# Kernel tuning notes

Hardware: AMD Instinct MI355X
Metric: run time of the kernel (lower is better)

Reference implementation:

```python
import jax, jax.numpy as jnp
import numpy as np

D_MODEL = 768
N_HEADS = 12
D_HEAD = D_MODEL // N_HEADS

def setup_inputs() -> dict:
    key = jax.random.key(0)
    ks = jax.random.split(key, 5)
    B, T = 2, 4096
    x = jax.random.normal(ks[0], (B, T, D_MODEL), dtype=jnp.float32)
    s_in = 1.0 / np.sqrt(D_MODEL)
    W_qkv = jax.random.normal(ks[1], (D_MODEL, 3 * D_MODEL), dtype=jnp.float32) * s_in
    b_qkv = jnp.zeros((3 * D_MODEL,), dtype=jnp.float32)
    W_proj = jax.random.normal(ks[2], (D_MODEL, D_MODEL), dtype=jnp.float32) * s_in
    b_proj = jnp.zeros((D_MODEL,), dtype=jnp.float32)
    return {"x": x, "W_qkv": W_qkv, "b_qkv": b_qkv, "W_proj": W_proj, "b_proj": b_proj}

def reference(x, W_qkv, b_qkv, W_proj, b_proj):
    B, T, C = x.shape
    qkv = x @ W_qkv + b_qkv                      # [B,T,3C]
    q, k, v = jnp.split(qkv, 3, axis=-1)
    def heads(t):
        return t.reshape(B, T, N_HEADS, D_HEAD).transpose(0, 2, 1, 3)  # [B,H,T,d]
    q, k, v = heads(q), heads(k), heads(v)
    scale = 1.0 / np.sqrt(D_HEAD)
    att = jnp.einsum('bhqd,bhkd->bhqk', q, k) * scale  # [B,H,T,T]
    causal = jnp.tril(jnp.ones((T, T), dtype=bool))
    att = jnp.where(causal[None, None], att, -jnp.inf)
    att = jax.nn.softmax(att, axis=-1)
    y = jnp.einsum('bhqk,bhkd->bhqd', att, v)          # [B,H,T,d]
    y = y.transpose(0, 2, 1, 3).reshape(B, T, C)
    return y @ W_proj + b_proj
```

## Files before the change

kernel.cpp:

```cpp
#include <hip/hip_runtime.h>
#include <hip/hip_bf16.h>

typedef __bf16 bf16_t;
typedef bf16_t bf16x4 __attribute__((ext_vector_type(4)));
typedef bf16_t bf16x8 __attribute__((ext_vector_type(8)));
typedef float  f32x4  __attribute__((ext_vector_type(4)));

#define TSEQ   4096
#define NBATCH 2
#define DMODEL 768
#define NHEADS 12
#define DHEAD  64
#define NTOK   (NBATCH*TSEQ)
#define NQKV   (3*DMODEL)

#define QSCALE 0.18033688011112042f
#define SMAX 24.0f

__device__ __forceinline__ f32x4 mfma16(bf16x8 a, bf16x8 b, f32x4 c) {
  return __builtin_amdgcn_mfma_f32_16x16x32_bf16(a, b, c, 0, 0, 0);
}

__device__ __forceinline__ void glds16(const bf16_t* g, bf16_t* l) {
  __builtin_amdgcn_global_load_lds(
      (const __attribute__((address_space(1))) void*)g,
      (__attribute__((address_space(3))) void*)l, 16, 0, 0);
}
__device__ __forceinline__ void glds16f(const float* g, float* l) {
  __builtin_amdgcn_global_load_lds(
      (const __attribute__((address_space(1))) void*)g,
      (__attribute__((address_space(3))) void*)l, 16, 0, 0);
}

__global__ __launch_bounds__(256) void k_transpose_cvt2(
    const float* __restrict__ W1, bf16_t* __restrict__ O1,
    const float* __restrict__ W2, bf16_t* __restrict__ O2) {
  __shared__ bf16_t tile[64][66];
  int t = blockIdx.x;
  const float* in; bf16_t* out; int R, C, c0, r0;
  if (t < 432) { in = W1; out = O1; R = DMODEL; C = NQKV;
                 c0 = (t % 36) * 64; r0 = (t / 36) * 64; }
  else { t -= 432; in = W2; out = O2; R = DMODEL; C = DMODEL;
         c0 = (t % 12) * 64; r0 = (t / 12) * 64; }
  const int tid = threadIdx.x;
  const int r = tid >> 2, cb = (tid & 3) * 16;
  const float* ip = in + (long)(r0 + r) * C + c0 + cb;
#pragma unroll
  for (int k = 0; k < 16; k += 4) {
    float4 v = *(const float4*)(ip + k);
    tile[r][cb + k + 0] = (bf16_t)v.x;
    tile[r][cb + k + 1] = (bf16_t)v.y;
    tile[r][cb + k + 2] = (bf16_t)v.z;
    tile[r][cb + k + 3] = (bf16_t)v.w;
  }
  __syncthreads();
  const int c = tid >> 2, rb = (tid & 3) * 16;
  bf16_t* op = out + (long)(c0 + c) * R + r0 + rb;
  bf16x8 v0, v1;
#pragma unroll
  for (int i = 0; i < 8; ++i) { v0[i] = tile[rb + i][c]; v1[i] = tile[rb + 8 + i][c]; }
  *(bf16x8*)(op) = v0;
  *(bf16x8*)(op + 8) = v1;
}

__global__ __launch_bounds__(256) void k_gemm_qkv(
    const float* __restrict__ X, const bf16_t* __restrict__ Bt,
    const float* __restrict__ bias,
    bf16_t* __restrict__ Qo, bf16_t* __restrict__ Ko, bf16_t* __restrict__ Vt) {
  __shared__ __align__(16) float  Asf[2 * 128 * 32];
  __shared__ __align__(16) bf16_t Bs[2 * 128 * 32];
  const int wave = threadIdx.x >> 6;
  const int lane = threadIdx.x & 63;
  const int quad = lane >> 4;
  const int l16  = lane & 15;
  const int m0 = blockIdx.x * 128;
  const int n0 = blockIdx.y * 128;

  const int arow = lane >> 3;
  const int achk = (lane & 7) ^ arow;
  const float* x0 = X + (long)(m0 + wave * 8 + arow) * DMODEL + achk * 4;
  const int srow = lane >> 2;
  const int scol = (lane & 3) * 8;
  const bf16_t* b0 = Bt + (long)(n0 + wave * 16 + srow) * DMODEL + scol;

  f32x4 acc[2][8] = {};

#pragma unroll
  for (int i = 0; i < 4; ++i)
    glds16f(x0 + (long)i * 32 * DMODEL, Asf + (i * 32 + wave * 8) * 32);
  glds16(b0,               Bs + wave * 16 * 32);
  glds16(b0 + 64 * DMODEL, Bs + (64 + wave * 16) * 32);
  __syncthreads();

  const int sk = l16 & 7;
  for (int ks = 0; ks < DMODEL / 32; ++ks) {
    const int p = ks & 1;
    if (ks + 1 < DMODEL / 32) {
      const int k1 = (ks + 1) * 32;
      float*  Asx = (p ? Asf : Asf + 128 * 32);
      bf16_t* Bsx = (p ? Bs : Bs + 128 * 32);
#pragma unroll
      for (int i = 0; i < 4; ++i)
        glds16f(x0 + (long)i * 32 * DMODEL + k1, Asx + (i * 32 + wave * 8) * 32);
      glds16(b0 + k1,               Bsx + wave * 16 * 32);
      glds16(b0 + 64 * DMODEL + k1, Bsx + (64 + wave * 16) * 32);
    }
    const float*  Ap = Asf + p * (128 * 32);
    const bf16_t* Bp = Bs + p * (128 * 32);

    const int r0 = wave * 32 + l16, r1 = r0 + 16;
    f32x4 a0lo = *(const f32x4*)(Ap + r0 * 32 + (((2 * quad)     ^ sk) << 2));
    f32x4 a0hi = *(const f32x4*)(Ap + r0 * 32 + (((2 * quad + 1) ^ sk) << 2));
    f32x4 a1lo = *(const f32x4*)(Ap + r1 * 32 + (((2 * quad)     ^ sk) << 2));
    f32x4 a1hi = *(const f32x4*)(Ap + r1 * 32 + (((2 * quad + 1) ^ sk) << 2));
    bf16x8 af0, af1;
#pragma unroll
    for (int j = 0; j < 4; ++j) {
      af0[j] = (bf16_t)a0lo[j]; af0[4 + j] = (bf16_t)a0hi[j];
      af1[j] = (bf16_t)a1lo[j]; af1[4 + j] = (bf16_t)a1hi[j];
    }
#pragma unroll
    for (int nt = 0; nt < 8; ++nt) {
      bf16x8 bfm = *(const bf16x8*)(Bp + (nt * 16 + l16) * 32 + quad * 8);
      acc[0][nt] = mfma16(af0, bfm, acc[0][nt]);
      acc[1][nt] = mfma16(af1, bfm, acc[1][nt]);
    }
    __syncthreads();
  }

#pragma unroll
  for (int s = 0; s < 2; ++s)
#pragma unroll
    for (int nt = 0; nt < 8; ++nt) {
      const int n = n0 + nt * 16 + l16;
      const float bv = bias[n];
      const int mb = m0 + wave * 32 + s * 16 + quad * 4;
      const int b = mb >> 12;
      const int t = mb & 4095;
      if (n < DMODEL) {
        const int h = n >> 6, d = n & 63;
        bf16_t* qp = Qo + (((long)(b * NHEADS + h) * TSEQ + t) << 6) + d;
#pragma unroll
        for (int j = 0; j < 4; ++j)
          qp[(long)j << 6] = (bf16_t)((acc[s][nt][j] + bv) * QSCALE);
      } else if (n < 2 * DMODEL) {
        const int n2 = n - DMODEL, h = n2 >> 6, d = n2 & 63;
        bf16_t* kp = Ko + (((long)(b * NHEADS + h) * TSEQ + t) << 6) + d;
#pragma unroll
        for (int j = 0; j < 4; ++j)
          kp[(long)j << 6] = (bf16_t)(acc[s][nt][j] + bv);
      } else {
        const int n2 = n - 2 * DMODEL, h = n2 >> 6, d = n2 & 63;
        bf16x4 v;
#pragma unroll
        for (int j = 0; j < 4; ++j) v[j] = (bf16_t)(acc[s][nt][j] + bv);
        *(bf16x4*)(Vt + ((long)(b * NHEADS + h) * DHEAD + d) * TSEQ + t) = v;
      }
    }
}

__global__ __launch_bounds__(256) void k_gemm_proj(
    const bf16_t* __restrict__ A, const bf16_t* __restrict__ Bt,
    const float* __restrict__ bias, float* __restrict__ out) {
  __shared__ __align__(16) bf16_t As[2 * 64 * 32];
  __shared__ __align__(16) bf16_t Bs[2 * 128 * 32];
  const int wave = threadIdx.x >> 6;
  const int lane = threadIdx.x & 63;
  const int quad = lane >> 4;
  const int l16  = lane & 15;
  const int m0 = blockIdx.x * 64;
  const int n0 = blockIdx.y * 128;

  const int srow = lane >> 2;
  const int scol = (lane & 3) * 8;
  const bf16_t* a0 = A + (long)(m0 + wave * 16 + srow) * DMODEL + scol;
  const bf16_t* b0 = Bt + (long)(n0 + wave * 16 + srow) * DMODEL + scol;

  f32x4 acc[8] = {};

  glds16(a0,               As + wave * 16 * 32);
  glds16(b0,               Bs + wave * 16 * 32);
  glds16(b0 + 64 * DMODEL, Bs + (64 + wave * 16) * 32);
  __syncthreads();

  for (int ks = 0; ks < DMODEL / 32; ++ks) {
    const int p = ks & 1;
    if (ks + 1 < DMODEL / 32) {
      const int k1 = (ks + 1) * 32;
      bf16_t* Asx = (p ? As : As + 64 * 32);
      bf16_t* Bsx = (p ? Bs : Bs + 128 * 32);
      glds16(a0 + k1,               Asx + wave * 16 * 32);
      glds16(b0 + k1,               Bsx + wave * 16 * 32);
      glds16(b0 + 64 * DMODEL + k1, Bsx + (64 + wave * 16) * 32);
    }
    const bf16_t* Ap = As + p * (64 * 32);
    const bf16_t* Bp = Bs + p * (128 * 32);

    bf16x8 af = *(const bf16x8*)(Ap + (wave * 16 + l16) * 32 + quad * 8);
#pragma unroll
    for (int nt = 0; nt < 8; ++nt) {
      bf16x8 bfm = *(const bf16x8*)(Bp + (nt * 16 + l16) * 32 + quad * 8);
      acc[nt] = mfma16(af, bfm, acc[nt]);
    }
    __syncthreads();
  }

#pragma unroll
  for (int nt = 0; nt < 8; ++nt) {
    const int n = n0 + nt * 16 + l16;
    const float bv = bias[n];
#pragma unroll
    for (int j = 0; j < 4; ++j) {
      const int m = m0 + wave * 16 + quad * 4 + j;
      out[(long)m * DMODEL + n] = acc[nt][j] + bv;
    }
  }
}

__global__ __launch_bounds__(256, 2) void k_attn(
    const bf16_t* __restrict__ Q, const bf16_t* __restrict__ K,
    const bf16_t* __restrict__ Vt,
    bf16_t* __restrict__ P0, bf16_t* __restrict__ P1,
    float* __restrict__ L0, float* __restrict__ L1) {
  __shared__ __align__(16) bf16_t kbuf[2][64 * 64];
  __shared__ __align__(16) bf16_t vbuf[2][64 * 64];
  const int wave = threadIdx.x >> 6;
  const int lane = threadIdx.x & 63;
  const int quad = lane >> 4;
  const int l16  = lane & 15;
  const int bh = blockIdx.x;
  const int qt = 15 - (blockIdx.y >> 1);
  const int sp = blockIdx.y & 1;
  const int half = 2 * qt + 2;
  const int c0 = sp ? half : 0;
  const int niter = half;
  bf16_t* Pp = sp ? P1 : P0;
  float*  Lp = sp ? L1 : L0;

  const bf16_t* Qh = Q + ((long)bh * TSEQ << 6);
  const bf16_t* Kh = K + ((long)bh * TSEQ << 6);
  const bf16_t* Vh = Vt + (long)bh * DHEAD * TSEQ;

  const int qbase = qt * 256 + wave * 64;

  bf16x8 qf[4][2];
#pragma unroll
  for (int s = 0; s < 4; ++s) {
    const bf16_t* qrow = Qh + ((long)(qbase + s * 16 + l16) << 6);
    qf[s][0] = *(const bf16x8*)(qrow + quad * 8);
    qf[s][1] = *(const bf16x8*)(qrow + 32 + quad * 8);
  }

  f32x4 acc[4][4] = {};
  float lS[4] = {0.f, 0.f, 0.f, 0.f};
  const f32x4 minit = {-SMAX, -SMAX, -SMAX, -SMAX};

  const int kperm = ((l16 >> 2) << 3) + (l16 & 3);
  const int swl = l16 & 7;
  const int srow = lane >> 3;
  const int cV = (lane & 7) ^ (srow & 7);
  const int cK0 = (lane & 7) ^ (srow & 3);
  const int cK1 = cK0 ^ 4;
  const int r0a = wave * 16, r0b = wave * 16 + 8;

  {
    const int k00 = c0 << 6;
    glds16(Kh + ((long)(k00 + r0a + srow) << 6) + cK0 * 8, &kbuf[0][r0a * 64]);
    glds16(Kh + ((long)(k00 + r0b + srow) << 6) + cK1 * 8, &kbuf[0][r0b * 64]);
    glds16(Vh + (long)(r0a + srow) * TSEQ + k00 + cV * 8,  &vbuf[0][r0a * 64]);
    glds16(Vh + (long)(r0b + srow) * TSEQ + k00 + cV * 8,  &vbuf[0][r0b * 64]);
  }
  __syncthreads();

  for (int ci = 0; ci < niter; ++ci) {
    const int p = ci & 1;
    const int k0 = (c0 + ci) << 6;
    if (ci + 1 < niter) {
      const int k1 = k0 + 64;
      glds16(Kh + ((long)(k1 + r0a + srow) << 6) + cK0 * 8, &kbuf[1 - p][r0a * 64]);
      glds16(Kh + ((long)(k1 + r0b + srow) << 6) + cK1 * 8, &kbuf[1 - p][r0b * 64]);
      glds16(Vh + (long)(r0a + srow) * TSEQ + k1 + cV * 8,  &vbuf[1 - p][r0a * 64]);
      glds16(Vh + (long)(r0b + srow) * TSEQ + k1 + cV * 8,  &vbuf[1 - p][r0b * 64]);
    }
    const bf16_t* kb = kbuf[p];
    const bf16_t* vb = vbuf[p];

#pragma unroll
    for (int g = 0; g < 2; ++g) {
      const int rw0 = (g * 32 + kperm) * 64;
      const int rw1 = (g * 32 + 4 + kperm) * 64;
      bf16x8 kf00 = *(const bf16x8*)(kb + rw0 + ((quad ^ swl) << 3));
      bf16x8 kf01 = *(const bf16x8*)(kb + rw0 + (((quad + 4) ^ swl) << 3));
      bf16x8 kf10 = *(const bf16x8*)(kb + rw1 + ((quad ^ swl) << 3));
      bf16x8 kf11 = *(const bf16x8*)(kb + rw1 + (((quad + 4) ^ swl) << 3));
      const bool domask = (k0 + g * 32 + 31 > qbase);

      bf16x8 pf[4];
#pragma unroll
      for (int s = 0; s < 4; ++s) {
        f32x4 st0 = minit, st1 = minit;
        st0 = mfma16(kf00, qf[s][0], st0);
        st0 = mfma16(kf01, qf[s][1], st0);
        st1 = mfma16(kf10, qf[s][0], st1);
        st1 = mfma16(kf11, qf[s][1], st1);
        if (domask) {
          const int qS = qbase + s * 16 + l16;
          const int kb0 = k0 + g * 32 + quad * 8;
#pragma unroll
          for (int j = 0; j < 4; ++j) {
            if (kb0 + j > qS)     st0[j] = -1e30f;
            if (kb0 + 4 + j > qS) st1[j] = -1e30f;
          }
        }
        float rs = 0.f;
#pragma unroll
        for (int j = 0; j < 4; ++j) {
          float e0 = __builtin_amdgcn_exp2f(st0[j]);
          float e1 = __builtin_amdgcn_exp2f(st1[j]);
          rs += e0 + e1;
          pf[s][j]     = (bf16_t)e0;
          pf[s][4 + j] = (bf16_t)e1;
        }
        lS[s] += rs;
      }
#pragma unroll
      for (int dt = 0; dt < 4; ++dt) {
        const int row = dt * 16 + l16;
        bf16x8 vf = *(const bf16x8*)(vb + row * 64 + ((((g << 2) + quad) ^ swl) << 3));
#pragma unroll
        for (int s = 0; s < 4; ++s)
          acc[s][dt] = mfma16(vf, pf[s], acc[s][dt]);
      }
    }
    __syncthreads();
  }

#pragma unroll
  for (int s = 0; s < 4; ++s) {
    lS[s] += __shfl_xor(lS[s], 16);
    lS[s] += __shfl_xor(lS[s], 32);
  }
#pragma unroll
  for (int s = 0; s < 4; ++s) {
    const int qS = qbase + s * 16 + l16;
    bf16_t* prow = Pp + (((long)bh * TSEQ + qS) << 6);
#pragma unroll
    for (int dt = 0; dt < 4; ++dt)
#pragma unroll
      for (int j = 0; j < 4; ++j)
        prow[dt * 16 + quad * 4 + j] = (bf16_t)acc[s][dt][j];
    if (quad == 0) Lp[(long)bh * TSEQ + qS] = lS[s];
  }
}

__global__ __launch_bounds__(256) void k_combine(
    const bf16_t* __restrict__ P0, const bf16_t* __restrict__ P1,
    const float* __restrict__ L0, const float* __restrict__ L1,
    bf16_t* __restrict__ Y) {
  const int f = (blockIdx.x * 256 + threadIdx.x) * 8;
  const int tok = f / DMODEL;
  const int c = f - tok * DMODEL;
  const int b = tok >> 12, q = tok & 4095;
  const int h = c >> 6, d0 = c & 63;
  const long bhq = (long)(b * NHEADS + h) * TSEQ + q;
  const long pidx = (bhq << 6) + d0;
  bf16x8 o0 = *(const bf16x8*)(P0 + pidx);
  bf16x8 o1 = *(const bf16x8*)(P1 + pidx);
  const float inv = 1.f / (L0[bhq] + L1[bhq]);
  bf16x8 r;
#pragma unroll
  for (int i = 0; i < 8; ++i) r[i] = (bf16_t)(((float)o0[i] + (float)o1[i]) * inv);
  *(bf16x8*)(Y + f) = r;
}

extern "C" void kernel_launch(void* const* d_in, const int* in_sizes, int n_in,
                              void* d_out, int out_size, void* d_ws, size_t ws_size,
                              hipStream_t stream) {
  (void)in_sizes; (void)n_in; (void)out_size; (void)ws_size;
  const float* x     = (const float*)d_in[0];
  const float* Wqkv  = (const float*)d_in[1];
  const float* bqkv  = (const float*)d_in[2];
  const float* Wproj = (const float*)d_in[3];
  const float* bproj = (const float*)d_in[4];
  float* out = (float*)d_out;

  char* ws = (char*)d_ws;
  bf16_t* wqkv_t  = (bf16_t*)ws; ws += (long)NQKV * DMODEL * 2;
  bf16_t* wproj_t = (bf16_t*)ws; ws += (long)DMODEL * DMODEL * 2;
  bf16_t* Qb      = (bf16_t*)ws; ws += (long)NTOK * DMODEL * 2;
  bf16_t* Kb      = (bf16_t*)ws; ws += (long)NTOK * DMODEL * 2;
  bf16_t* Vtb     = (bf16_t*)ws; ws += (long)NTOK * DMODEL * 2;
  bf16_t* Sb      = (bf16_t*)ws; ws += (long)NTOK * DMODEL * 2;
  bf16_t* P0b     = (bf16_t*)ws; ws += (long)NTOK * DMODEL * 2;
  bf16_t* P1b     = (bf16_t*)ws; ws += (long)NTOK * DMODEL * 2;
  float*  L0b     = (float*)ws;  ws += (long)NHEADS * NBATCH * TSEQ * 4;
  float*  L1b     = (float*)ws;  ws += (long)NHEADS * NBATCH * TSEQ * 4;

  k_transpose_cvt2<<<576, 256, 0, stream>>>(Wqkv, wqkv_t, Wproj, wproj_t);
  k_gemm_qkv<<<dim3(NTOK / 128, NQKV / 128), 256, 0, stream>>>(x, wqkv_t, bqkv, Qb, Kb, Vtb);
  k_attn<<<dim3(NBATCH * NHEADS, 32), 256, 0, stream>>>(Qb, Kb, Vtb, P0b, P1b, L0b, L1b);
  k_combine<<<(NTOK * DMODEL) / (256 * 8), 256, 0, stream>>>(P0b, P1b, L0b, L1b, Sb);
  k_gemm_proj<<<dim3(NTOK / 64, DMODEL / 128), 256, 0, stream>>>(Sb, wproj_t, bproj, out);
}
```

Before: 236.0 us.

## Fuse split-attention combine into projection GEMM A-operand load

Removes the separate combine kernel. The projection GEMM now loads both partial attention outputs (P0, P1) straight from the head-major layout, precomputes per-row 1/(L0+L1) in LDS, and merges them while building the A fragment. This drops one launch and the write and re-read of the combined Y buffer, at the cost of doubling A-tile loads and doing the merge arithmetic once per N-tile block (six times redundantly). It also vectorizes the attention partial-output stores to bf16x4.

```diff
diff --git a/kernel.cpp b/kernel.cpp
--- a/kernel.cpp
+++ b/kernel.cpp
@@ -160,25 +160,41 @@
 }
 
 __global__ __launch_bounds__(256) void k_gemm_proj(
-    const bf16_t* __restrict__ A, const bf16_t* __restrict__ Bt,
-    const float* __restrict__ bias, float* __restrict__ out) {
-  __shared__ __align__(16) bf16_t As[2 * 64 * 32];
+    const bf16_t* __restrict__ P0, const bf16_t* __restrict__ P1,
+    const float* __restrict__ L0, const float* __restrict__ L1,
+    const bf16_t* __restrict__ Bt, const float* __restrict__ bias,
+    float* __restrict__ out) {
+  __shared__ __align__(16) bf16_t A0s[2 * 64 * 32];
+  __shared__ __align__(16) bf16_t A1s[2 * 64 * 32];
   __shared__ __align__(16) bf16_t Bs[2 * 128 * 32];
+  __shared__ float linv[NHEADS * 64];
   const int wave = threadIdx.x >> 6;
   const int lane = threadIdx.x & 63;
   const int quad = lane >> 4;
   const int l16  = lane & 15;
   const int m0 = blockIdx.x * 64;
   const int n0 = blockIdx.y * 128;
+  const int b  = m0 >> 12;
+  const int t0 = m0 & 4095;
+
+  for (int i = threadIdx.x; i < NHEADS * 64; i += 256) {
+    const int h = i >> 6, t = i & 63;
+    const long idx = (long)(b * NHEADS + h) * TSEQ + t0 + t;
+    linv[i] = 1.f / (L0[idx] + L1[idx]);
+  }
 
   const int srow = lane >> 2;
   const int scol = (lane & 3) * 8;
-  const bf16_t* a0 = A + (long)(m0 + wave * 16 + srow) * DMODEL + scol;
   const bf16_t* b0 = Bt + (long)(n0 + wave * 16 + srow) * DMODEL + scol;
+  const long arowbase = (long)(t0 + wave * 16 + srow);
 
   f32x4 acc[8] = {};
 
-  glds16(a0,               As + wave * 16 * 32);
+  {
+    const long off = (((long)(b * NHEADS + 0) * TSEQ + arowbase) << 6) + scol;
+    glds16(P0 + off, A0s + wave * 16 * 32);
+    glds16(P1 + off, A1s + wave * 16 * 32);
+  }
   glds16(b0,               Bs + wave * 16 * 32);
   glds16(b0 + 64 * DMODEL, Bs + (64 + wave * 16) * 32);
   __syncthreads();
@@ -187,16 +203,28 @@
     const int p = ks & 1;
     if (ks + 1 < DMODEL / 32) {
       const int k1 = (ks + 1) * 32;
-      bf16_t* Asx = (p ? As : As + 64 * 32);
+      const int ksn = ks + 1;
+      bf16_t* A0x = (p ? A0s : A0s + 64 * 32);
+      bf16_t* A1x = (p ? A1s : A1s + 64 * 32);
       bf16_t* Bsx = (p ? Bs : Bs + 128 * 32);
-      glds16(a0 + k1,               Asx + wave * 16 * 32);
+      const long off = (((long)(b * NHEADS + (ksn >> 1)) * TSEQ + arowbase) << 6)
+                       + ((ksn & 1) << 5) + scol;
+      glds16(P0 + off, A0x + wave * 16 * 32);
+      glds16(P1 + off, A1x + wave * 16 * 32);
       glds16(b0 + k1,               Bsx + wave * 16 * 32);
       glds16(b0 + 64 * DMODEL + k1, Bsx + (64 + wave * 16) * 32);
     }
-    const bf16_t* Ap = As + p * (64 * 32);
-    const bf16_t* Bp = Bs + p * (128 * 32);
-
-    bf16x8 af = *(const bf16x8*)(Ap + (wave * 16 + l16) * 32 + quad * 8);
+    const bf16_t* A0p = A0s + p * (64 * 32);
+    const bf16_t* A1p = A1s + p * (64 * 32);
+    const bf16_t* Bp  = Bs + p * (128 * 32);
+
+    bf16x8 a0 = *(const bf16x8*)(A0p + (wave * 16 + l16) * 32 + quad * 8);
+    bf16x8 a1 = *(const bf16x8*)(A1p + (wave * 16 + l16) * 32 + quad * 8);
+    const float li = linv[(ks >> 1) * 64 + wave * 16 + l16];
+    bf16x8 af;
+#pragma unroll
+    for (int j = 0; j < 8; ++j)
+      af[j] = (bf16_t)(((float)a0[j] + (float)a1[j]) * li);
 #pragma unroll
     for (int nt = 0; nt < 8; ++nt) {
       bf16x8 bfm = *(const bf16x8*)(Bp + (nt * 16 + l16) * 32 + quad * 8);
@@ -345,32 +373,14 @@
     const int qS = qbase + s * 16 + l16;
     bf16_t* prow = Pp + (((long)bh * TSEQ + qS) << 6);
 #pragma unroll
-    for (int dt = 0; dt < 4; ++dt)
-#pragma unroll
-      for (int j = 0; j < 4; ++j)
-        prow[dt * 16 + quad * 4 + j] = (bf16_t)acc[s][dt][j];
+    for (int dt = 0; dt < 4; ++dt) {
+      bf16x4 w;
+#pragma unroll
+      for (int j = 0; j < 4; ++j) w[j] = (bf16_t)acc[s][dt][j];
+      *(bf16x4*)(prow + dt * 16 + quad * 4) = w;
+    }
     if (quad == 0) Lp[(long)bh * TSEQ + qS] = lS[s];
   }
-}
-
-__global__ __launch_bounds__(256) void k_combine(
-    const bf16_t* __restrict__ P0, const bf16_t* __restrict__ P1,
-    const float* __restrict__ L0, const float* __restrict__ L1,
-    bf16_t* __restrict__ Y) {
-  const int f = (blockIdx.x * 256 + threadIdx.x) * 8;
-  const int tok = f / DMODEL;
-  const int c = f - tok * DMODEL;
-  const int b = tok >> 12, q = tok & 4095;
-  const int h = c >> 6, d0 = c & 63;
-  const long bhq = (long)(b * NHEADS + h) * TSEQ + q;
-  const long pidx = (bhq << 6) + d0;
-  bf16x8 o0 = *(const bf16x8*)(P0 + pidx);
-  bf16x8 o1 = *(const bf16x8*)(P1 + pidx);
-  const float inv = 1.f / (L0[bhq] + L1[bhq]);
-  bf16x8 r;
-#pragma unroll
-  for (int i = 0; i < 8; ++i) r[i] = (bf16_t)(((float)o0[i] + (float)o1[i]) * inv);
-  *(bf16x8*)(Y + f) = r;
 }
 
 extern "C" void kernel_launch(void* const* d_in, const int* in_sizes, int n_in,
@@ -390,7 +400,6 @@
   bf16_t* Qb      = (bf16_t*)ws; ws += (long)NTOK * DMODEL * 2;
   bf16_t* Kb      = (bf16_t*)ws; ws += (long)NTOK * DMODEL * 2;
   bf16_t* Vtb     = (bf16_t*)ws; ws += (long)NTOK * DMODEL * 2;
-  bf16_t* Sb      = (bf16_t*)ws; ws += (long)NTOK * DMODEL * 2;
   bf16_t* P0b     = (bf16_t*)ws; ws += (long)NTOK * DMODEL * 2;
   bf16_t* P1b     = (bf16_t*)ws; ws += (long)NTOK * DMODEL * 2;
   float*  L0b     = (float*)ws;  ws += (long)NHEADS * NBATCH * TSEQ * 4;
@@ -399,6 +408,6 @@
   k_transpose_cvt2<<<576, 256, 0, stream>>>(Wqkv, wqkv_t, Wproj, wproj_t);
   k_gemm_qkv<<<dim3(NTOK / 128, NQKV / 128), 256, 0, stream>>>(x, wqkv_t, bqkv, Qb, Kb, Vtb);
   k_attn<<<dim3(NBATCH * NHEADS, 32), 256, 0, stream>>>(Qb, Kb, Vtb, P0b, P1b, L0b, L1b);
-  k_combine<<<(NTOK * DMODEL) / (256 * 8), 256, 0, stream>>>(P0b, P1b, L0b, L1b, Sb);
-  k_gemm_proj<<<dim3(NTOK / 64, DMODEL / 128), 256, 0, stream>>>(Sb, wproj_t, bproj, out);
-}
+  k_gemm_proj<<<dim3(NTOK / 64, DMODEL / 128), 256, 0, stream>>>(
+      P0b, P1b, L0b, L1b, wproj_t, bproj, out);
+}
```

Result: faster. 226.6 us (median of 2 runs) (-4.0%).
